# Kernel optimization log

Hardware: AMD Instinct MI355X
Metric: run time of the kernel (lower is better)

The kernel has to match this reference:

```python
import jax, jax.numpy as jnp
import numpy as np

INPUT_SIZE = 256
OUTPUT_SIZE = 128
N = 8192
SLOPE = 0.01
NEG_BIG = -9e15


def setup_inputs() -> dict:
    key = jax.random.key(0)
    k_h, k_adj, k_W, k_a = jax.random.split(key, 4)
    h = jax.random.normal(k_h, (N, INPUT_SIZE), dtype=jnp.float32)
    adj = jax.random.randint(k_adj, (N, N), 0, 2, dtype=jnp.int32)
    # xavier_uniform with gain=1.414
    gain = 1.414
    lim_W = gain * np.sqrt(6.0 / (INPUT_SIZE + OUTPUT_SIZE))
    W = jax.random.uniform(k_W, (INPUT_SIZE, OUTPUT_SIZE), dtype=jnp.float32, minval=-lim_W, maxval=lim_W)
    lim_a = gain * np.sqrt(6.0 / (2 * OUTPUT_SIZE + 1))
    a = jax.random.uniform(k_a, (2 * OUTPUT_SIZE, 1), dtype=jnp.float32, minval=-lim_a, maxval=lim_a)
    return {"h": h, "adj": adj, "W": W, "a": a}


def reference(h, adj, W, a):
    # Wh: [N, F]
    Wh = h @ W
    Fo = Wh.shape[1]
    # Original builds [N, N, 2F] concat then matmul with a; equivalent to
    # e[i, j] = leaky_relu(Wh[i] . a[:F] + Wh[j] . a[F:]) via broadcasting.
    src = Wh @ a[:Fo, 0]   # [N]
    dst = Wh @ a[Fo:, 0]   # [N]
    e = jax.nn.leaky_relu(src[:, None] + dst[None, :], negative_slope=SLOPE)  # [N, N]
    att = jnp.where(adj > 0, e, NEG_BIG)
    att = jax.nn.softmax(att, axis=1)
    return att @ Wh
```

## Files before the change

kernel.cpp:

```cpp
#include <hip/hip_runtime.h>
#include <hip/hip_bf16.h>

typedef unsigned short u16;
typedef unsigned int u32;
typedef __attribute__((ext_vector_type(8))) short short8;
typedef __attribute__((ext_vector_type(4))) float f32x4;

#define NN 8192
#define KIN 256
#define FOUT 128
#define SPLITS 8
#define KPER (NN / SPLITS)
#define KSTEPS (KPER / 32)
#define L2E 1.4426950408889634f

__device__ __forceinline__ float exp2fast(float x) { return __builtin_amdgcn_exp2f(x); }

__device__ __forceinline__ u16 f2bf(float f) {
    u32 u = __float_as_uint(f);
    u32 r = ((u >> 16) & 1u) + 0x7fffu;
    return (u16)((u + r) >> 16);
}
__device__ __forceinline__ u32 pk_bf16(float a, float b) {
    union { __hip_bfloat162 h2; u32 u; } cv;
    cv.h2 = __float22bfloat162_rn(make_float2(a, b));
    return cv.u;
}
__device__ __forceinline__ u32 fkey(float f) {
    u32 b = __float_as_uint(f);
    return (b & 0x80000000u) ? ~b : (b | 0x80000000u);
}
__device__ __forceinline__ float funkey(u32 k) {
    u32 b = (k & 0x80000000u) ? (k & 0x7fffffffu) : ~k;
    return __uint_as_float(b);
}

__global__ __launch_bounds__(512) void k1_wh(
    const float* __restrict__ h, const float* __restrict__ W, const float* __restrict__ a,
    u16* __restrict__ whfrag,
    float* __restrict__ src, float* __restrict__ dl2e, u32* __restrict__ gmaxk)
{
    __shared__ float hT[64][36];
    __shared__ u16   lt[128][40];
    __shared__ float sd[32][2];
    const int t  = threadIdx.x;
    const int m0 = blockIdx.x * 32;
    const int rq = t >> 5, cq = t & 31;

    float acc[2][4];
#pragma unroll
    for (int i = 0; i < 2; i++)
#pragma unroll
        for (int j = 0; j < 4; j++) acc[i][j] = 0.f;
    if (t < 64) sd[t >> 1][t & 1] = 0.f;

    for (int kt = 0; kt < KIN; kt += 64) {
        __syncthreads();
        {
            int r = t >> 4, kc = (t & 15) * 4;
            float4 hv = *(const float4*)(h + (size_t)(m0 + r) * KIN + kt + kc);
            hT[kc + 0][r] = hv.x; hT[kc + 1][r] = hv.y;
            hT[kc + 2][r] = hv.z; hT[kc + 3][r] = hv.w;
        }
        __syncthreads();
        for (int k = 0; k < 64; k++) {
            float4 wv = *(const float4*)(W + (size_t)(kt + k) * FOUT + cq * 4);
            float h0 = hT[k][rq * 2 + 0], h1 = hT[k][rq * 2 + 1];
            acc[0][0] += h0 * wv.x; acc[0][1] += h0 * wv.y; acc[0][2] += h0 * wv.z; acc[0][3] += h0 * wv.w;
            acc[1][0] += h1 * wv.x; acc[1][1] += h1 * wv.y; acc[1][2] += h1 * wv.z; acc[1][3] += h1 * wv.w;
        }
    }
#pragma unroll
    for (int i = 0; i < 2; i++) {
        int row = rq * 2 + i;
        float sp = 0.f, dp = 0.f;
#pragma unroll
        for (int j = 0; j < 4; j++) {
            sp += acc[i][j] * a[cq * 4 + j];
            dp += acc[i][j] * a[FOUT + cq * 4 + j];
            lt[cq * 4 + j][row] = f2bf(acc[i][j]);
        }
        atomicAdd(&sd[row][0], sp);
        atomicAdd(&sd[row][1], dp);
    }
    __syncthreads();
    if (t < 32) { src[m0 + t] = sd[t][0]; dl2e[m0 + t] = sd[t][1] * L2E; }
    if (t < 64) {
        float v = (t < 32) ? sd[t][1] : -3.0e38f;
#pragma unroll
        for (int off = 32; off >= 1; off >>= 1) v = fmaxf(v, __shfl_down(v, off));
        if (t == 0) atomicMax(gmaxk, fkey(v));
    }
    const int kstep = blockIdx.x;
    {
        int nt = t >> 6;
        int l  = t & 63;
        short8 v = *(const short8*)&lt[nt * 16 + (l & 15)][(l >> 4) * 8];
        *(short8*)(whfrag + ((size_t)(kstep * 8 + nt) * 64 + l) * 8) = v;
    }
}

__global__ __launch_bounds__(512, 4) void k2_attn(
    const int* __restrict__ adj, const float* __restrict__ src, const float* __restrict__ dl2e,
    const u16* __restrict__ whfrag, const u32* __restrict__ gmaxk,
    float* __restrict__ accp, float* __restrict__ lp)
{
    const int t = threadIdx.x;
    const int lane = t & 63, wave = t >> 6;
    const int strip = blockIdx.x * 8 + wave;
    const int i0 = strip * 16;
    const int split = blockIdx.y;
    const int l15 = lane & 15;
    const int kq = (lane >> 4) * 8;

    float sp = src[i0 + l15] * L2E;
    float gm = funkey(*gmaxk) * L2E;
    float xx = sp + gm;
    float C = fmaxf(xx, 0.01f * xx);
    const float y1 = sp - C, y2 = 0.01f * sp - C;

    const int* arow = adj + (size_t)(i0 + l15) * NN;
    const int st0 = blockIdx.x & (KSTEPS - 1);
    const int kbase = split * KPER;

    f32x4 acc[8];
#pragma unroll
    for (int nt = 0; nt < 8; nt++) acc[nt] = {0.f, 0.f, 0.f, 0.f};
    float psum = 0.f;

    int4 aL[2], aH[2]; float4 dL[2], dH[2];
#pragma unroll
    for (int s = 0; s < 2; s++) {
        int kb = kbase + ((st0 + s) & (KSTEPS - 1)) * 32;
        aL[s] = *(const int4*)(arow + kb + kq);
        aH[s] = *(const int4*)(arow + kb + kq + 4);
        dL[s] = *(const float4*)(dl2e + kb + kq);
        dH[s] = *(const float4*)(dl2e + kb + kq + 4);
    }

#pragma unroll 4
    for (int it = 0; it < KSTEPS; ++it) {
        const int sl = it & 1;
        const int kb = kbase + ((st0 + it) & (KSTEPS - 1)) * 32;

        uint4 bv[8];
        const u16* wf = whfrag + ((size_t)(kb >> 5) * 8 * 64 + lane) * 8;
#pragma unroll
        for (int nt = 0; nt < 8; nt++)
            bv[nt] = *(const uint4*)(wf + (size_t)nt * 64 * 8);

        int4 al = aL[sl], ah = aH[sl];
        float4 dl = dL[sl], dh = dH[sl];
        float p0, p1, p2, p3, p4, p5, p6, p7;
        {
            float x;
            x = fmaxf(y1 + dl.x, y2 + 0.01f * dl.x); p0 = exp2fast(al.x > 0 ? x : -1.0e9f);
            x = fmaxf(y1 + dl.y, y2 + 0.01f * dl.y); p1 = exp2fast(al.y > 0 ? x : -1.0e9f);
            x = fmaxf(y1 + dl.z, y2 + 0.01f * dl.z); p2 = exp2fast(al.z > 0 ? x : -1.0e9f);
            x = fmaxf(y1 + dl.w, y2 + 0.01f * dl.w); p3 = exp2fast(al.w > 0 ? x : -1.0e9f);
            x = fmaxf(y1 + dh.x, y2 + 0.01f * dh.x); p4 = exp2fast(ah.x > 0 ? x : -1.0e9f);
            x = fmaxf(y1 + dh.y, y2 + 0.01f * dh.y); p5 = exp2fast(ah.y > 0 ? x : -1.0e9f);
            x = fmaxf(y1 + dh.z, y2 + 0.01f * dh.z); p6 = exp2fast(ah.z > 0 ? x : -1.0e9f);
            x = fmaxf(y1 + dh.w, y2 + 0.01f * dh.w); p7 = exp2fast(ah.w > 0 ? x : -1.0e9f);
        }
        psum += ((p0 + p1) + (p2 + p3)) + ((p4 + p5) + (p6 + p7));
        union { short8 s8; u32 u[4]; } af;
        af.u[0] = pk_bf16(p0, p1); af.u[1] = pk_bf16(p2, p3);
        af.u[2] = pk_bf16(p4, p5); af.u[3] = pk_bf16(p6, p7);

        {
            int kb2 = kbase + ((st0 + it + 2) & (KSTEPS - 1)) * 32;
            aL[sl] = *(const int4*)(arow + kb2 + kq);
            aH[sl] = *(const int4*)(arow + kb2 + kq + 4);
            dL[sl] = *(const float4*)(dl2e + kb2 + kq);
            dH[sl] = *(const float4*)(dl2e + kb2 + kq + 4);
        }

#pragma unroll
        for (int nt = 0; nt < 8; nt++) {
            union { uint4 q; short8 s8; } bf; bf.q = bv[nt];
            acc[nt] = __builtin_amdgcn_mfma_f32_16x16x32_bf16(af.s8, bf.s8, acc[nt], 0, 0, 0);
        }
    }

    float v = psum;
    v += __shfl_down(v, 32);
    v += __shfl_down(v, 16);
    if (lane < 16) lp[split * NN + i0 + lane] = v;

    float* ab2 = accp + (size_t)split * (NN * FOUT);
#pragma unroll
    for (int nt = 0; nt < 8; nt++)
        *(f32x4*)&ab2[((size_t)(strip * 8 + nt) * 64 + lane) * 4] = acc[nt];
}

__global__ __launch_bounds__(256) void k2b_rsum(const float* __restrict__ lp,
                                               float* __restrict__ rinv)
{
    int i = blockIdx.x * 256 + threadIdx.x;
    float s = 0.f;
#pragma unroll
    for (int sp = 0; sp < SPLITS; sp++) s += lp[sp * NN + i];
    rinv[i] = 1.0f / s;
}

__global__ __launch_bounds__(256) void k3_comb(
    const float* __restrict__ accp, const float* __restrict__ rinv, float* __restrict__ out)
{
    int idx = blockIdx.x * 256 + threadIdx.x;
    int tile = idx >> 6, l = idx & 63;
    float4 s = make_float4(0.f, 0.f, 0.f, 0.f);
#pragma unroll
    for (int sp = 0; sp < SPLITS; sp++) {
        float4 v = *(const float4*)(accp + (size_t)sp * (NN * FOUT) + (size_t)idx * 4);
        s.x += v.x; s.y += v.y; s.z += v.z; s.w += v.w;
    }
    int row0 = (tile >> 3) * 16 + (l >> 4) * 4;
    int col  = (tile & 7) * 16 + (l & 15);
    float4 ri = *(const float4*)(rinv + row0);
    out[(size_t)(row0 + 0) * FOUT + col] = s.x * ri.x;
    out[(size_t)(row0 + 1) * FOUT + col] = s.y * ri.y;
    out[(size_t)(row0 + 2) * FOUT + col] = s.z * ri.z;
    out[(size_t)(row0 + 3) * FOUT + col] = s.w * ri.w;
}

extern "C" void kernel_launch(void* const* d_in, const int* in_sizes, int n_in,
                              void* d_out, int out_size, void* d_ws, size_t ws_size,
                              hipStream_t stream) {
    const float* h   = (const float*)d_in[0];
    const int*   adj = (const int*)d_in[1];
    const float* W   = (const float*)d_in[2];
    const float* a   = (const float*)d_in[3];
    float* out = (float*)d_out;

    char* ws = (char*)d_ws;
    u16*   whfrag = (u16*)ws;
    float* src    = (float*)(ws + (2u << 20));
    float* dl2e   = src + NN;
    u32*   gmaxk  = (u32*)(dl2e + NN);
    float* accp   = (float*)(ws + (3u << 20));
    float* lp     = (float*)(ws + (35u << 20));
    float* rinv   = (float*)(ws + (36u << 20));

    (void)hipMemsetAsync(gmaxk, 0, sizeof(u32), stream);
    k1_wh<<<dim3(NN / 32), dim3(512), 0, stream>>>(h, W, a, whfrag, src, dl2e, gmaxk);
    k2_attn<<<dim3(NN / 128, SPLITS), dim3(512), 0, stream>>>(adj, src, dl2e, whfrag, gmaxk, accp, lp);
    k2b_rsum<<<dim3(NN / 256), dim3(256), 0, stream>>>(lp, rinv);
    k3_comb<<<dim3((NN * FOUT / 4) / 256), dim3(256), 0, stream>>>(accp, rinv, out);
}
```

Before: 433.2 us.

## Process two 16-row strips per wave to reuse Wh fragment loads

Each wave now handles 32 rows (two 16-row MFMA strips), so every loaded Wh B-fragment and dl2e vector feeds two accumulator sets. Blocks shrink to 256 threads (4 waves) with the same grid, keeping total rows covered. This halves global/L2 traffic for whfrag per output row but doubles accumulator registers and lowers the occupancy hint, which may reduce latency hiding for the adjacency stream.

```diff
diff --git a/kernel.cpp b/kernel.cpp
--- a/kernel.cpp
+++ b/kernel.cpp
@@ -100,42 +100,45 @@
     }
 }
 
-__global__ __launch_bounds__(512, 4) void k2_attn(
+__global__ __launch_bounds__(256, 2) void k2_attn(
     const int* __restrict__ adj, const float* __restrict__ src, const float* __restrict__ dl2e,
     const u16* __restrict__ whfrag, const u32* __restrict__ gmaxk,
     float* __restrict__ accp, float* __restrict__ lp)
 {
     const int t = threadIdx.x;
     const int lane = t & 63, wave = t >> 6;
-    const int strip = blockIdx.x * 8 + wave;
-    const int i0 = strip * 16;
+    const int strip2 = blockIdx.x * 4 + wave;
+    const int i0 = strip2 * 32;
     const int split = blockIdx.y;
     const int l15 = lane & 15;
     const int kq = (lane >> 4) * 8;
 
-    float sp = src[i0 + l15] * L2E;
+    float sp0 = src[i0 + l15] * L2E;
+    float sp1 = src[i0 + 16 + l15] * L2E;
     float gm = funkey(*gmaxk) * L2E;
-    float xx = sp + gm;
-    float C = fmaxf(xx, 0.01f * xx);
-    const float y1 = sp - C, y2 = 0.01f * sp - C;
-
-    const int* arow = adj + (size_t)(i0 + l15) * NN;
+    float x0 = sp0 + gm, x1 = sp1 + gm;
+    float C0 = fmaxf(x0, 0.01f * x0), C1 = fmaxf(x1, 0.01f * x1);
+    const float y1a = sp0 - C0, y2a = 0.01f * sp0 - C0;
+    const float y1b = sp1 - C1, y2b = 0.01f * sp1 - C1;
+
+    const int* arow0 = adj + (size_t)(i0 + l15) * NN;
+    const int* arow1 = adj + (size_t)(i0 + 16 + l15) * NN;
     const int st0 = blockIdx.x & (KSTEPS - 1);
     const int kbase = split * KPER;
 
-    f32x4 acc[8];
-#pragma unroll
-    for (int nt = 0; nt < 8; nt++) acc[nt] = {0.f, 0.f, 0.f, 0.f};
-    float psum = 0.f;
-
-    int4 aL[2], aH[2]; float4 dL[2], dH[2];
+    f32x4 acc0[8], acc1[8];
+#pragma unroll
+    for (int nt = 0; nt < 8; nt++) { acc0[nt] = {0.f, 0.f, 0.f, 0.f}; acc1[nt] = {0.f, 0.f, 0.f, 0.f}; }
+    float psum0 = 0.f, psum1 = 0.f;
+
+    int4 a0L[2], a0H[2], a1L[2], a1H[2];
 #pragma unroll
     for (int s = 0; s < 2; s++) {
         int kb = kbase + ((st0 + s) & (KSTEPS - 1)) * 32;
-        aL[s] = *(const int4*)(arow + kb + kq);
-        aH[s] = *(const int4*)(arow + kb + kq + 4);
-        dL[s] = *(const float4*)(dl2e + kb + kq);
-        dH[s] = *(const float4*)(dl2e + kb + kq + 4);
+        a0L[s] = *(const int4*)(arow0 + kb + kq);
+        a0H[s] = *(const int4*)(arow0 + kb + kq + 4);
+        a1L[s] = *(const int4*)(arow1 + kb + kq);
+        a1H[s] = *(const int4*)(arow1 + kb + kq + 4);
     }
 
 #pragma unroll 4
@@ -149,49 +152,79 @@
         for (int nt = 0; nt < 8; nt++)
             bv[nt] = *(const uint4*)(wf + (size_t)nt * 64 * 8);
 
-        int4 al = aL[sl], ah = aH[sl];
-        float4 dl = dL[sl], dh = dH[sl];
-        float p0, p1, p2, p3, p4, p5, p6, p7;
+        const float4 dl = *(const float4*)(dl2e + kb + kq);
+        const float4 dh = *(const float4*)(dl2e + kb + kq + 4);
+
+        int4 al = a0L[sl], ah = a0H[sl];
+        float q0, q1, q2, q3, q4, q5, q6, q7;
         {
             float x;
-            x = fmaxf(y1 + dl.x, y2 + 0.01f * dl.x); p0 = exp2fast(al.x > 0 ? x : -1.0e9f);
-            x = fmaxf(y1 + dl.y, y2 + 0.01f * dl.y); p1 = exp2fast(al.y > 0 ? x : -1.0e9f);
-            x = fmaxf(y1 + dl.z, y2 + 0.01f * dl.z); p2 = exp2fast(al.z > 0 ? x : -1.0e9f);
-            x = fmaxf(y1 + dl.w, y2 + 0.01f * dl.w); p3 = exp2fast(al.w > 0 ? x : -1.0e9f);
-            x = fmaxf(y1 + dh.x, y2 + 0.01f * dh.x); p4 = exp2fast(ah.x > 0 ? x : -1.0e9f);
-            x = fmaxf(y1 + dh.y, y2 + 0.01f * dh.y); p5 = exp2fast(ah.y > 0 ? x : -1.0e9f);
-            x = fmaxf(y1 + dh.z, y2 + 0.01f * dh.z); p6 = exp2fast(ah.z > 0 ? x : -1.0e9f);
-            x = fmaxf(y1 + dh.w, y2 + 0.01f * dh.w); p7 = exp2fast(ah.w > 0 ? x : -1.0e9f);
-        }
-        psum += ((p0 + p1) + (p2 + p3)) + ((p4 + p5) + (p6 + p7));
-        union { short8 s8; u32 u[4]; } af;
-        af.u[0] = pk_bf16(p0, p1); af.u[1] = pk_bf16(p2, p3);
-        af.u[2] = pk_bf16(p4, p5); af.u[3] = pk_bf16(p6, p7);
+            x = fmaxf(y1a + dl.x, y2a + 0.01f * dl.x); q0 = exp2fast(al.x > 0 ? x : -1.0e9f);
+            x = fmaxf(y1a + dl.y, y2a + 0.01f * dl.y); q1 = exp2fast(al.y > 0 ? x : -1.0e9f);
+            x = fmaxf(y1a + dl.z, y2a + 0.01f * dl.z); q2 = exp2fast(al.z > 0 ? x : -1.0e9f);
+            x = fmaxf(y1a + dl.w, y2a + 0.01f * dl.w); q3 = exp2fast(al.w > 0 ? x : -1.0e9f);
+            x = fmaxf(y1a + dh.x, y2a + 0.01f * dh.x); q4 = exp2fast(ah.x > 0 ? x : -1.0e9f);
+            x = fmaxf(y1a + dh.y, y2a + 0.01f * dh.y); q5 = exp2fast(ah.y > 0 ? x : -1.0e9f);
+            x = fmaxf(y1a + dh.z, y2a + 0.01f * dh.z); q6 = exp2fast(ah.z > 0 ? x : -1.0e9f);
+            x = fmaxf(y1a + dh.w, y2a + 0.01f * dh.w); q7 = exp2fast(ah.w > 0 ? x : -1.0e9f);
+        }
+        psum0 += ((q0 + q1) + (q2 + q3)) + ((q4 + q5) + (q6 + q7));
+        union { short8 s8; u32 u[4]; } af0;
+        af0.u[0] = pk_bf16(q0, q1); af0.u[1] = pk_bf16(q2, q3);
+        af0.u[2] = pk_bf16(q4, q5); af0.u[3] = pk_bf16(q6, q7);
+
+        al = a1L[sl]; ah = a1H[sl];
+        {
+            float x;
+            x = fmaxf(y1b + dl.x, y2b + 0.01f * dl.x); q0 = exp2fast(al.x > 0 ? x : -1.0e9f);
+            x = fmaxf(y1b + dl.y, y2b + 0.01f * dl.y); q1 = exp2fast(al.y > 0 ? x : -1.0e9f);
+            x = fmaxf(y1b + dl.z, y2b + 0.01f * dl.z); q2 = exp2fast(al.z > 0 ? x : -1.0e9f);
+            x = fmaxf(y1b + dl.w, y2b + 0.01f * dl.w); q3 = exp2fast(al.w > 0 ? x : -1.0e9f);
+            x = fmaxf(y1b + dh.x, y2b + 0.01f * dh.x); q4 = exp2fast(ah.x > 0 ? x : -1.0e9f);
+            x = fmaxf(y1b + dh.y, y2b + 0.01f * dh.y); q5 = exp2fast(ah.y > 0 ? x : -1.0e9f);
+            x = fmaxf(y1b + dh.z, y2b + 0.01f * dh.z); q6 = exp2fast(ah.z > 0 ? x : -1.0e9f);
+            x = fmaxf(y1b + dh.w, y2b + 0.01f * dh.w); q7 = exp2fast(ah.w > 0 ? x : -1.0e9f);
+        }
+        psum1 += ((q0 + q1) + (q2 + q3)) + ((q4 + q5) + (q6 + q7));
+        union { short8 s8; u32 u[4]; } af1;
+        af1.u[0] = pk_bf16(q0, q1); af1.u[1] = pk_bf16(q2, q3);
+        af1.u[2] = pk_bf16(q4, q5); af1.u[3] = pk_bf16(q6, q7);
 
         {
             int kb2 = kbase + ((st0 + it + 2) & (KSTEPS - 1)) * 32;
-            aL[sl] = *(const int4*)(arow + kb2 + kq);
-            aH[sl] = *(const int4*)(arow + kb2 + kq + 4);
-            dL[sl] = *(const float4*)(dl2e + kb2 + kq);
-            dH[sl] = *(const float4*)(dl2e + kb2 + kq + 4);
+            a0L[sl] = *(const int4*)(arow0 + kb2 + kq);
+            a0H[sl] = *(const int4*)(arow0 + kb2 + kq + 4);
+            a1L[sl] = *(const int4*)(arow1 + kb2 + kq);
+            a1H[sl] = *(const int4*)(arow1 + kb2 + kq + 4);
         }
 
 #pragma unroll
         for (int nt = 0; nt < 8; nt++) {
             union { uint4 q; short8 s8; } bf; bf.q = bv[nt];
-            acc[nt] = __builtin_amdgcn_mfma_f32_16x16x32_bf16(af.s8, bf.s8, acc[nt], 0, 0, 0);
-        }
-    }
-
-    float v = psum;
-    v += __shfl_down(v, 32);
-    v += __shfl_down(v, 16);
-    if (lane < 16) lp[split * NN + i0 + lane] = v;
+            acc0[nt] = __builtin_amdgcn_mfma_f32_16x16x32_bf16(af0.s8, bf.s8, acc0[nt], 0, 0, 0);
+            acc1[nt] = __builtin_amdgcn_mfma_f32_16x16x32_bf16(af1.s8, bf.s8, acc1[nt], 0, 0, 0);
+        }
+    }
+
+    float v0 = psum0;
+    v0 += __shfl_down(v0, 32);
+    v0 += __shfl_down(v0, 16);
+    float v1 = psum1;
+    v1 += __shfl_down(v1, 32);
+    v1 += __shfl_down(v1, 16);
+    if (lane < 16) {
+        lp[split * NN + i0 + lane] = v0;
+        lp[split * NN + i0 + 16 + lane] = v1;
+    }
 
     float* ab2 = accp + (size_t)split * (NN * FOUT);
+    const int s16a = strip2 * 2, s16b = strip2 * 2 + 1;
 #pragma unroll
     for (int nt = 0; nt < 8; nt++)
-        *(f32x4*)&ab2[((size_t)(strip * 8 + nt) * 64 + lane) * 4] = acc[nt];
+        *(f32x4*)&ab2[((size_t)(s16a * 8 + nt) * 64 + lane) * 4] = acc0[nt];
+#pragma unroll
+    for (int nt = 0; nt < 8; nt++)
+        *(f32x4*)&ab2[((size_t)(s16b * 8 + nt) * 64 + lane) * 4] = acc1[nt];
 }
 
 __global__ __launch_bounds__(256) void k2b_rsum(const float* __restrict__ lp,
@@ -244,7 +277,7 @@
 
     (void)hipMemsetAsync(gmaxk, 0, sizeof(u32), stream);
     k1_wh<<<dim3(NN / 32), dim3(512), 0, stream>>>(h, W, a, whfrag, src, dl2e, gmaxk);
-    k2_attn<<<dim3(NN / 128, SPLITS), dim3(512), 0, stream>>>(adj, src, dl2e, whfrag, gmaxk, accp, lp);
+    k2_attn<<<dim3(NN / 128, SPLITS), dim3(256), 0, stream>>>(adj, src, dl2e, whfrag, gmaxk, accp, lp);
     k2b_rsum<<<dim3(NN / 256), dim3(256), 0, stream>>>(lp, rinv);
     k3_comb<<<dim3((NN * FOUT / 4) / 256), dim3(256), 0, stream>>>(accp, rinv, out);
 }
```

Result: faster. 421.7 us (median of 2 runs) (-2.7%).
